# Optimization experiments

Measured on AMD Instinct MI355X. Metric: run time of the kernel, lower is better.

## Reference

```python
import jax, jax.numpy as jnp
import numpy as np

F = 8        # number of fields
N_SEQ = 2    # first N_SEQ fields are sequence features
B = 4096     # batch
L = 50       # sequence length for sequence fields
V = 100000   # vocab per field
E = 64       # emb_dim


def setup_inputs() -> dict:
    key = jax.random.key(0)
    k1, k2, k3 = jax.random.split(key, 3)
    x_seq = jax.random.randint(k1, (N_SEQ, B, L), 0, V)          # sequence field inputs
    x_cat = jax.random.randint(k2, (F - N_SEQ, B, 1), 0, V)      # categorical field inputs
    # packed pair-wise tables: tables[a, t] is the embedding table for field a
    # when interacting with target field t (diagonal a==t is unused).
    # RandomNormal(stddev=0.01) initializer in the original.
    tables = jax.random.normal(k3, (F, F, V, E), dtype=jnp.float32) * 0.01
    return {"x_seq": x_seq, "x_cat": x_cat, "tables": tables}


def _pooled(tables, x_seq, x_cat):
    # P[a, t] in [B, E]: field a's input embedded with table (a -> t),
    # mean-pooled over the sequence axis (keepdims semantics folded in).
    P = []
    for a in range(F):  # small fixed loop over fields (structurally distinct inputs)
        idx = x_seq[a] if a < N_SEQ else x_cat[a - N_SEQ]   # [B, La]
        emb = jnp.take(tables[a], idx, axis=1)              # [F, B, La, E]
        P.append(emb.mean(axis=2))                          # [F, B, E]
    return jnp.stack(P)                                     # [F(src), F(tgt), B, E]


def reference(x_seq, x_cat, tables):
    P = _pooled(tables, x_seq, x_cat)
    iu, ju = np.triu_indices(F, k=1)  # all unordered field pairs (a < b)
    # sum over pairs of <emb_{a->b}(x_a), emb_{b->a}(x_b)>
    out = jnp.einsum('pbe,pbe->b', P[iu, ju], P[ju, iu])     # [B]
    return out[:, None, None]                                # [B, 1, 1], matching tf.matmul output
```

## Files before the change

kernel.cpp:

```cpp
#include <hip/hip_runtime.h>

#define FQ 8
#define NSEQ 2
#define BQ 4096
#define LQ 50
#define VQ 100000
#define EQ 64

__global__ __launch_bounds__(256, 4) void ffl_kernel(
    const int* __restrict__ x_seq,
    const int* __restrict__ x_cat,
    const float* __restrict__ tables,
    float* __restrict__ out)
{
    const int b    = blockIdx.x;
    const int tid  = threadIdx.x;
    const int lane = tid & 63;
    const int wave = tid >> 6;

    __shared__ float P[FQ][FQ][EQ];
    __shared__ int   s_idx[NSEQ * LQ];
    __shared__ int   c_idx[FQ - NSEQ];
    __shared__ float partial[4];

    if (tid < NSEQ * LQ) {
        int a = tid / LQ;
        int l = tid - a * LQ;
        s_idx[tid] = x_seq[(a * BQ + b) * LQ + l];
    } else if (tid < NSEQ * LQ + (FQ - NSEQ)) {
        int a = tid - NSEQ * LQ;
        c_idx[a] = x_cat[a * BQ + b];
    }
    __syncthreads();

    for (int p = wave; p < FQ * (FQ - 1); p += 4) {
        int a = p / (FQ - 1);
        int r = p - a * (FQ - 1);
        int t = r + (r >= a ? 1 : 0);
        const float* __restrict__ tab = tables + (size_t)(a * FQ + t) * VQ * EQ;
        float acc;
        if (a < NSEQ) {
            acc = 0.0f;
            #pragma unroll 5
            for (int l = 0; l < LQ; ++l) {
                int v = s_idx[a * LQ + l];
                acc += tab[(size_t)v * EQ + lane];
            }
            acc *= (1.0f / LQ);
        } else {
            int v = c_idx[a - NSEQ];
            acc = tab[(size_t)v * EQ + lane];
        }
        P[a][t][lane] = acc;
    }
    __syncthreads();

    float sum = 0.0f;
    {
        int p = 0;
        #pragma unroll
        for (int a = 0; a < FQ; ++a) {
            #pragma unroll
            for (int c = a + 1; c < FQ; ++c) {
                if ((p & 3) == wave)
                    sum += P[a][c][lane] * P[c][a][lane];
                ++p;
            }
        }
    }
    #pragma unroll
    for (int off = 32; off > 0; off >>= 1)
        sum += __shfl_down(sum, off, 64);
    if (lane == 0) partial[wave] = sum;
    __syncthreads();
    if (tid == 0)
        out[b] = partial[0] + partial[1] + partial[2] + partial[3];
}

extern "C" void kernel_launch(void* const* d_in, const int* in_sizes, int n_in,
                              void* d_out, int out_size, void* d_ws, size_t ws_size,
                              hipStream_t stream) {
    const int*   x_seq  = (const int*)d_in[0];
    const int*   x_cat  = (const int*)d_in[1];
    const float* tables = (const float*)d_in[2];
    float*       out    = (float*)d_out;
    ffl_kernel<<<BQ, 256, 0, stream>>>(x_seq, x_cat, tables, out);
}
```

Measured before the change: 119.9 us.

## Split work per field pair across blocks with separate pair-reduction kernel

Each block now handles a single field pair for four batch rows, computing both pooled embeddings and their dot product, instead of one block per batch row doing all 56 gathers. Partial results per pair are written to workspace and summed by a second kernel, with an atomic fallback when workspace is small. This is meant to spread the uneven sequence-gather work across many blocks and raise memory-level parallelism, at the cost of an extra launch and partial buffer traffic.

```diff
diff --git a/kernel.cpp b/kernel.cpp
--- a/kernel.cpp
+++ b/kernel.cpp
@@ -6,75 +6,99 @@
 #define LQ 50
 #define VQ 100000
 #define EQ 64
+#define NPAIR 28
+#define CQ 4
+#define CHUNKS (BQ / CQ)
 
-__global__ __launch_bounds__(256, 4) void ffl_kernel(
+__device__ const int PA[NPAIR] = {0,0,0,0,0,0,0, 1,1,1,1,1,1, 2,2,2,2,2, 3,3,3,3, 4,4,4, 5,5, 6};
+__device__ const int PB[NPAIR] = {1,2,3,4,5,6,7, 2,3,4,5,6,7, 3,4,5,6,7, 4,5,6,7, 5,6,7, 6,7, 7};
+
+template <bool ATOMIC>
+__global__ __launch_bounds__(256) void pair_pool_dot(
     const int* __restrict__ x_seq,
     const int* __restrict__ x_cat,
     const float* __restrict__ tables,
+    float* __restrict__ partial,
     float* __restrict__ out)
 {
-    const int b    = blockIdx.x;
+    const int blk   = blockIdx.x;
+    const int pair  = blk / CHUNKS;
+    const int chunk = blk - pair * CHUNKS;
+    const int b0    = chunk * CQ;
+    const int a = PA[pair], c = PB[pair];
     const int tid  = threadIdx.x;
     const int lane = tid & 63;
     const int wave = tid >> 6;
+    const int b    = b0 + wave;
 
-    __shared__ float P[FQ][FQ][EQ];
-    __shared__ int   s_idx[NSEQ * LQ];
-    __shared__ int   c_idx[FQ - NSEQ];
-    __shared__ float partial[4];
+    __shared__ int sidx[2][CQ][LQ];
 
-    if (tid < NSEQ * LQ) {
-        int a = tid / LQ;
-        int l = tid - a * LQ;
-        s_idx[tid] = x_seq[(a * BQ + b) * LQ + l];
-    } else if (tid < NSEQ * LQ + (FQ - NSEQ)) {
-        int a = tid - NSEQ * LQ;
-        c_idx[a] = x_cat[a * BQ + b];
-    }
-    __syncthreads();
-
-    for (int p = wave; p < FQ * (FQ - 1); p += 4) {
-        int a = p / (FQ - 1);
-        int r = p - a * (FQ - 1);
-        int t = r + (r >= a ? 1 : 0);
-        const float* __restrict__ tab = tables + (size_t)(a * FQ + t) * VQ * EQ;
-        float acc;
-        if (a < NSEQ) {
-            acc = 0.0f;
-            #pragma unroll 5
-            for (int l = 0; l < LQ; ++l) {
-                int v = s_idx[a * LQ + l];
-                acc += tab[(size_t)v * EQ + lane];
-            }
-            acc *= (1.0f / LQ);
-        } else {
-            int v = c_idx[a - NSEQ];
-            acc = tab[(size_t)v * EQ + lane];
-        }
-        P[a][t][lane] = acc;
-    }
-    __syncthreads();
-
-    float sum = 0.0f;
-    {
-        int p = 0;
-        #pragma unroll
-        for (int a = 0; a < FQ; ++a) {
-            #pragma unroll
-            for (int c = a + 1; c < FQ; ++c) {
-                if ((p & 3) == wave)
-                    sum += P[a][c][lane] * P[c][a][lane];
-                ++p;
-            }
+    if (a < NSEQ) {
+        if (tid < CQ * LQ) {
+            int bl = tid / LQ, l = tid - bl * LQ;
+            sidx[0][bl][l] = x_seq[((size_t)a * BQ + b0 + bl) * LQ + l];
         }
     }
+    if (c < NSEQ) {
+        if (tid < CQ * LQ) {
+            int bl = tid / LQ, l = tid - bl * LQ;
+            sidx[1][bl][l] = x_seq[((size_t)c * BQ + b0 + bl) * LQ + l];
+        }
+    }
+    if (a < NSEQ || c < NSEQ) __syncthreads();
+
+    const float* __restrict__ tab1 = tables + ((size_t)a * FQ + c) * VQ * EQ;
+    const float* __restrict__ tab2 = tables + ((size_t)c * FQ + a) * VQ * EQ;
+
+    float va, vc;
+    if (a < NSEQ) {
+        float acc = 0.0f;
+        #pragma unroll 10
+        for (int l = 0; l < LQ; ++l)
+            acc += tab1[(size_t)sidx[0][wave][l] * EQ + lane];
+        va = acc * (1.0f / LQ);
+    } else {
+        int v = x_cat[(size_t)(a - NSEQ) * BQ + b];
+        va = tab1[(size_t)v * EQ + lane];
+    }
+    if (c < NSEQ) {
+        float acc = 0.0f;
+        #pragma unroll 10
+        for (int l = 0; l < LQ; ++l)
+            acc += tab2[(size_t)sidx[1][wave][l] * EQ + lane];
+        vc = acc * (1.0f / LQ);
+    } else {
+        int v = x_cat[(size_t)(c - NSEQ) * BQ + b];
+        vc = tab2[(size_t)v * EQ + lane];
+    }
+
+    float prod = va * vc;
     #pragma unroll
-    for (int off = 32; off > 0; off >>= 1)
-        sum += __shfl_down(sum, off, 64);
-    if (lane == 0) partial[wave] = sum;
-    __syncthreads();
-    if (tid == 0)
-        out[b] = partial[0] + partial[1] + partial[2] + partial[3];
+    for (int off = 32; off; off >>= 1)
+        prod += __shfl_down(prod, off, 64);
+    if (lane == 0) {
+        if (ATOMIC) atomicAdd(&out[b], prod);
+        else        partial[(size_t)pair * BQ + b] = prod;
+    }
+}
+
+__global__ __launch_bounds__(256) void reduce_pairs(
+    const float* __restrict__ partial, float* __restrict__ out)
+{
+    int b = blockIdx.x * 256 + threadIdx.x;
+    if (b < BQ) {
+        float s = 0.0f;
+        #pragma unroll
+        for (int p = 0; p < NPAIR; ++p)
+            s += partial[(size_t)p * BQ + b];
+        out[b] = s;
+    }
+}
+
+__global__ __launch_bounds__(256) void zero_out(float* __restrict__ out)
+{
+    int b = blockIdx.x * 256 + threadIdx.x;
+    if (b < BQ) out[b] = 0.0f;
 }
 
 extern "C" void kernel_launch(void* const* d_in, const int* in_sizes, int n_in,
@@ -84,5 +108,16 @@
     const int*   x_cat  = (const int*)d_in[1];
     const float* tables = (const float*)d_in[2];
     float*       out    = (float*)d_out;
-    ffl_kernel<<<BQ, 256, 0, stream>>>(x_seq, x_cat, tables, out);
+
+    const size_t need = (size_t)NPAIR * BQ * sizeof(float);
+    if (ws_size >= need) {
+        float* partial = (float*)d_ws;
+        pair_pool_dot<false><<<NPAIR * CHUNKS, 256, 0, stream>>>(
+            x_seq, x_cat, tables, partial, out);
+        reduce_pairs<<<(BQ + 255) / 256, 256, 0, stream>>>(partial, out);
+    } else {
+        zero_out<<<(BQ + 255) / 256, 256, 0, stream>>>(out);
+        pair_pool_dot<true><<<NPAIR * CHUNKS, 256, 0, stream>>>(
+            x_seq, x_cat, tables, nullptr, out);
+    }
 }
```

Result: no change. 119.4 us (-0.4%).
